# Performance work log

Measured on AMD Instinct MI355X. Metric: run time of the kernel, lower is better.

## Reference

```python
import jax, jax.numpy as jnp
import numpy as np

MAX_REL = 7  # maxRelativeDist

def _rel_pos_table(L, max_rel):
    # |i-j|, with distances beyond max_rel mapped to max_rel + log2(d - max_rel), clipped to [0, 2*max_rel]
    idx = jnp.arange(L)
    d = jnp.abs(idx[:, None] - idx[None, :]).astype(jnp.float32)
    far = d > max_rel
    d = jnp.where(far, max_rel + jnp.log2(jnp.maximum(d - max_rel, 1.0)), d)
    return jnp.clip(d, 0, 2 * max_rel).astype(jnp.int32)  # [L, L]

def setup_inputs() -> dict:
    key = jax.random.key(0)
    ks = jax.random.split(key, 16)
    B, L, C, P, H, DK = 8, 2048, 512, 64, 8, 64
    s = 0.02
    inp = {
        'qx': jax.random.normal(ks[0], (B, L, C), jnp.float32),
        'kx': jax.random.normal(ks[1], (B, L, C), jnp.float32),
        'vx': jax.random.normal(ks[2], (B, L, C), jnp.float32),
        'maskPAD': jnp.ones((B, L, L), jnp.int32),
        # pseudoAttn: Linear(C, P)
        'Wp': jax.random.normal(ks[3], (C, P), jnp.float32) * s,
        'bp': jnp.zeros((P,), jnp.float32),
        # WQ/WK: Linear(C, dkEnhance*DK*H) with dkEnhance=1
        'Wq': jax.random.normal(ks[4], (C, H * DK), jnp.float32) * s,
        'bq': jnp.zeros((H * DK,), jnp.float32),
        'Wk': jax.random.normal(ks[5], (C, H * DK), jnp.float32) * s,
        'bk': jnp.zeros((H * DK,), jnp.float32),
        'Wv': jax.random.normal(ks[6], (C, H * DK), jnp.float32) * s,
        'bv': jnp.zeros((H * DK,), jnp.float32),
        'Wo': jax.random.normal(ks[7], (H * DK, C), jnp.float32) * s,
        'bo': jnp.zeros((C,), jnp.float32),
        # relative position embeddings: [2*MAX_REL+1, H]
        'embK': jax.random.normal(ks[8], (2 * MAX_REL + 1, H), jnp.float32) * s,
        'embB': jax.random.normal(ks[9], (2 * MAX_REL + 1, H), jnp.float32) * s,
    }
    return inp

def reference(qx, kx, vx, maskPAD, Wp, bp, Wq, bq, Wk, bk, Wv, bv, Wo, bo, embK, embB):
    # dropout is identity (eval mode); preScores=None
    B, L, C = qx.shape
    H = embK.shape[1]
    DK = Wv.shape[1] // H
    P = Wp.shape[1]

    # pseudo-token compression
    pScore = vx @ Wp + bp                                   # [B, L, P]
    mask = (maskPAD[:, 0] == 0)[:, :, None]                 # [B, L, 1]
    pScore = jnp.where(mask, jnp.float32(-2.0 ** 15), pScore)
    pAlpha = jax.nn.softmax(pScore, axis=1)                 # softmax over L
    kxc = jnp.einsum('blp,blc->bpc', pAlpha, kx)            # [B, P, C]
    vxc = jnp.einsum('blp,blc->bpc', pAlpha, vx)            # [B, P, C]
    pAlpha_d = jax.lax.stop_gradient(pAlpha)

    # multi-head projections
    q = (qx @ Wq + bq).reshape(B, L, H, DK)                 # [B, L, H, DK]
    k = (kxc @ Wk + bk).reshape(B, P, H, DK)
    v = (vxc @ Wv + bv).reshape(B, P, H, DK)

    scores = jnp.einsum('blhd,bphd->bhlp', q, k) / np.sqrt(DK)  # [B, H, L, P]

    # relative-position modulation
    relTab = _rel_pos_table(L, MAX_REL)                     # [L, L] int
    Kmat = jnp.transpose(embK[relTab], (2, 1, 0))           # [H, L, L]
    Bmat = jnp.transpose(embB[relTab], (2, 1, 0))           # [H, L, L]
    Kterm = jnp.einsum('hlm,bmp->bhlp', Kmat, pAlpha_d)
    Bterm = jnp.einsum('hlm,bmp->bhlp', Bmat, pAlpha_d)
    scores = scores * Kterm + Bterm

    alpha = jax.nn.softmax(scores, axis=3)                  # over pseudo tokens
    z = jnp.einsum('bhlp,bphd->blhd', alpha, v).reshape(B, L, H * DK)
    z = z @ Wo + bo                                         # [B, L, C]
    return z, pScore, scores
```

## Files before the change

kernel.cpp:

```cpp
#include <hip/hip_runtime.h>


typedef __attribute__((ext_vector_type(8))) short bhalf8;
typedef __attribute__((ext_vector_type(4))) float fx4;

__device__ __forceinline__ unsigned short f2bf(float f) {
  union { float f; unsigned u; } v; v.f = f;
  unsigned u = v.u + 0x7fffu + ((v.u >> 16) & 1u);
  return (unsigned short)(u >> 16);
}
__device__ __forceinline__ float bf2f(unsigned short h) {
  union { unsigned u; float f; } v; v.u = ((unsigned)h) << 16;
  return v.f;
}
__device__ __forceinline__ void gld16(const void* g, void* l) {
  __builtin_amdgcn_global_load_lds(
      (const __attribute__((address_space(1))) void*)g,
      (__attribute__((address_space(3))) void*)l, 16, 0, 0);
}

template <int BM, int BN, int CMODE, int AF32, int KSPLIT>
__device__ __forceinline__ void gemm_body(
    int bxx, int byy, int bzz, char* smemc,
    const void* __restrict__ Av, const unsigned short* __restrict__ BT,
    const float* __restrict__ bias, void* __restrict__ Cout,
    int K, int lda, int ldbt, int ldc, int HDIV,
    long sAb, long sAh, long sBb, long sBh, long sCb, long sCh, long sCk,
    const int* __restrict__ mpad, float* __restrict__ aux)
{
  constexpr int NA = BM / 16, NB = BN / 16, NT = NA + NB;
  constexpr int WM = BM / 2, WN = BN / 2, FM = WM / 16, FN = WN / 16;
  unsigned short* lds = (unsigned short*)smemc;
  const int t = threadIdx.x, l = t & 63, w = t >> 6;
  const int wr = w >> 1, wc = w & 1;
  const int zz = bzz, b = zz / HDIV, h = zz % HDIV;
  const int row0 = KSPLIT ? 0 : byy * BM;
  const int koff = KSPLIT ? byy * K : 0;
  const long cko = KSPLIT ? (long)byy * sCk : 0;
  const int col0 = bxx * BN;
  const unsigned short* Ag = (const unsigned short*)Av + b * sAb + h * sAh + (long)row0 * lda + koff;
  const float* AgF = (const float*)Av + b * sAb + h * sAh + (long)row0 * lda + koff;
  const unsigned short* Bg = BT + b * sBb + h * sBh + (long)col0 * ldbt + koff;
  const int lr = l & 15, lc = l >> 4;

  fx4 acc[FM][FN];
#pragma unroll
  for (int i = 0; i < FM; ++i)
#pragma unroll
    for (int j = 0; j < FN; ++j) acc[i][j] = fx4{0.f, 0.f, 0.f, 0.f};

  for (int k0 = 0; k0 < K; k0 += 32) {
#pragma unroll
    for (int i = 0; i < NT / 4; ++i) {
      const int tile = w + i * 4;
      if constexpr (AF32 == 1) {
        if (tile < NA) {
          const float* gf = AgF + (long)(tile * 16 + lr) * lda + k0 + lc * 8;
          float4 x = *(const float4*)gf, y = *(const float4*)(gf + 4);
          bhalf8 pk;
          pk[0] = (short)f2bf(x.x); pk[1] = (short)f2bf(x.y);
          pk[2] = (short)f2bf(x.z); pk[3] = (short)f2bf(x.w);
          pk[4] = (short)f2bf(y.x); pk[5] = (short)f2bf(y.y);
          pk[6] = (short)f2bf(y.z); pk[7] = (short)f2bf(y.w);
          *(bhalf8*)&lds[tile * 512 + l * 8] = pk;
        } else {
          gld16(Bg + (long)((tile - NA) * 16 + lr) * ldbt + k0 + lc * 8, &lds[tile * 512]);
        }
      } else if constexpr (AF32 == 2) {
        if (tile < NA) {
          const float* gf = (const float*)Av + (long)zz * sAb + (long)byy * 131072
                            + (long)(tile * 16 + lr) * 512 + k0 + lc * 8;
          float4 x = make_float4(0.f, 0.f, 0.f, 0.f), y = x;
#pragma unroll
          for (int c = 0; c < 4; ++c) {
            float4 a = *(const float4*)(gf + (long)c * 32768);
            float4 bq = *(const float4*)(gf + (long)c * 32768 + 4);
            x.x += a.x; x.y += a.y; x.z += a.z; x.w += a.w;
            y.x += bq.x; y.y += bq.y; y.z += bq.z; y.w += bq.w;
          }
          bhalf8 pk;
          pk[0] = (short)f2bf(x.x); pk[1] = (short)f2bf(x.y);
          pk[2] = (short)f2bf(x.z); pk[3] = (short)f2bf(x.w);
          pk[4] = (short)f2bf(y.x); pk[5] = (short)f2bf(y.y);
          pk[6] = (short)f2bf(y.z); pk[7] = (short)f2bf(y.w);
          *(bhalf8*)&lds[tile * 512 + l * 8] = pk;
        } else {
          gld16(Bg + (long)((tile - NA) * 16 + lr) * ldbt + k0 + lc * 8, &lds[tile * 512]);
        }
      } else {
        const unsigned short* g = (tile < NA)
            ? Ag + (long)(tile * 16 + lr) * lda + k0 + lc * 8
            : Bg + (long)((tile - NA) * 16 + lr) * ldbt + k0 + lc * 8;
        gld16(g, &lds[tile * 512]);
      }
    }
    __syncthreads();
    bhalf8 af[FM], bf[FN];
#pragma unroll
    for (int i = 0; i < FM; ++i) af[i] = *(const bhalf8*)&lds[(wr * FM + i) * 512 + l * 8];
#pragma unroll
    for (int j = 0; j < FN; ++j) bf[j] = *(const bhalf8*)&lds[(NA + wc * FN + j) * 512 + l * 8];
#pragma unroll
    for (int i = 0; i < FM; ++i)
#pragma unroll
      for (int j = 0; j < FN; ++j)
        acc[i][j] = __builtin_amdgcn_mfma_f32_16x16x32_bf16(af[i], bf[j], acc[i][j], 0, 0, 0);
    __syncthreads();
  }

  if constexpr (CMODE == 3) {
    float (*tbuf)[65] = (float(*)[65])(smemc + NT * 1024);
#pragma unroll
    for (int fm = 0; fm < FM; ++fm) {
#pragma unroll
      for (int fn = 0; fn < FN; ++fn) {
        const int rg0 = row0 + wr * WM + fm * 16 + lc * 4;
        const int cg = col0 + wc * WN + fn * 16 + lr;
        const float bb = bias[cg];
#pragma unroll
        for (int jj = 0; jj < 4; ++jj) {
          const int rg = rg0 + jj;
          float vv = acc[fm][fn][jj] + bb;
          if (mpad[((long)(rg >> 11)) * (2048L * 2048) + (rg & 2047)] == 0) vv = -32768.f;
          __builtin_nontemporal_store(vv, (float*)Cout + (long)rg * ldc + cg);
          tbuf[rg - row0][cg] = vv;
        }
      }
    }
    __syncthreads();
    const int b0 = row0 >> 11, l0b = row0 & 2047;
    const int pp = t >> 2, li0 = (t & 3) * 16;
    float* dst = aux + ((long)b0 * 64 + pp) * 2048 + l0b + li0;
#pragma unroll
    for (int i = 0; i < 16; i += 4) {
      float4 o = make_float4(tbuf[li0 + i][pp],     tbuf[li0 + i + 1][pp],
                             tbuf[li0 + i + 2][pp], tbuf[li0 + i + 3][pp]);
      *(float4*)(dst + i) = o;
    }
  } else {
#pragma unroll
    for (int fm = 0; fm < FM; ++fm) {
#pragma unroll
      for (int fn = 0; fn < FN; ++fn) {
        const int rg0 = row0 + wr * WM + fm * 16 + lc * 4;
        const int cg = col0 + wc * WN + fn * 16 + lr;
        float bb = 0.f;
        if constexpr (CMODE == 4) {
          bb = (zz == 0) ? bias[cg] : ((const float*)mpad)[cg];
        } else {
          bb = bias ? bias[cg] : 0.f;
        }
#pragma unroll
        for (int jj = 0; jj < 4; ++jj) {
          const int rg = rg0 + jj;
          const float v = acc[fm][fn][jj] + bb;
          if constexpr (CMODE == 0) {
            ((float*)Cout)[b * sCb + h * sCh + cko + (long)rg * ldc + cg] = v;
          } else if constexpr (CMODE == 1) {
            ((unsigned short*)Cout)[b * sCb + h * sCh + (long)rg * ldc + cg] = f2bf(v);
          } else if constexpr (CMODE == 2) {
            ((unsigned short*)Cout)[(((long)(rg >> 6) * 8 + (cg >> 6)) * 64 + (cg & 63)) * 64 + (rg & 63)] = f2bf(v);
          } else if constexpr (CMODE == 4) {
            if (zz == 0)
              ((unsigned short*)Cout)[(long)rg * ldc + cg] = f2bf(v);
            else
              ((unsigned short*)Cout)[262144 + (((long)(rg >> 6) * 8 + (cg >> 6)) * 64 + (cg & 63)) * 64 + (rg & 63)] = f2bf(v);
          } else {
            __builtin_nontemporal_store(v, (float*)Cout + b * sCb + h * sCh + cko + (long)rg * ldc + cg);
          }
        }
      }
    }
  }
}

template <int BM, int BN, int CMODE, int AF32, int KSPLIT>
__global__ __launch_bounds__(256)
void gemm_mfma(const void* __restrict__ Av, const unsigned short* __restrict__ BT,
               const float* __restrict__ bias, void* __restrict__ Cout,
               int K, int lda, int ldbt, int ldc, int HDIV,
               long sAb, long sAh, long sBb, long sBh, long sCb, long sCh, long sCk,
               const int* __restrict__ mpad, float* __restrict__ aux)
{
  constexpr int SM = (BM / 16 + BN / 16) * 1024 + (CMODE == 3 ? 16640 : 0);
  __shared__ __align__(16) char smem[SM];
  gemm_body<BM, BN, CMODE, AF32, KSPLIT>(blockIdx.x, blockIdx.y, blockIdx.z, smem,
      Av, BT, bias, Cout, K, lda, ldbt, ldc, HDIV,
      sAb, sAh, sBb, sBh, sCb, sCh, sCk, mpad, aux);
}

__device__ __forceinline__ void kb_body(int bx, int by, char* smemc,
    const unsigned short* __restrict__ PSb,
    const float* __restrict__ embK, const float* __restrict__ embB,
    ushort2* __restrict__ KB)
{
  const int L = 2048, STR = 338;
  unsigned short* psw = (unsigned short*)smemc;
  float (*eKs)[8] = (float(*)[8])(smemc + 43264);
  float (*eBs)[8] = (float(*)[8])(smemc + 43264 + 512);
  const int t = threadIdx.x, b = by, l0 = bx * 64;
  if (t < 128) {
    int r = t >> 3, h = t & 7;
    eKs[r][h] = (r < 15) ? embK[r * 8 + h] : 0.f;
    eBs[r][h] = (r < 15) ? embB[r * 8 + h] : 0.f;
  }
  const int W0 = l0 - 136;
  const int w = t >> 6, ln = t & 63;
  for (int pr = w * 16; pr < w * 16 + 16; ++pr) {
    const unsigned short* src = PSb + ((long)b * 64 + pr) * 2048;
#pragma unroll
    for (int pass = 0; pass < 6; ++pass) {
      int j = pass * 64 + ln;
      if (j < 337) {
        int g = (j == 336) ? (L - 1) : (W0 + j);
        g = g < 0 ? 0 : (g > L - 1 ? L - 1 : g);
        psw[pr * STR + j] = src[g];
      }
    }
  }
  __syncthreads();
  const int p = ln;
  const int Btab[14] = {0,1,2,3,4,5,6,8,10,14,22,38,70,134};
  for (int step = 0; step < 16; ++step) {
    const int l = l0 + w * 16 + step;
    float U[15];
#pragma unroll
    for (int r = 0; r < 14; ++r) {
      int hi = l + Btab[r]; hi = hi > L - 1 ? L - 1 : hi;
      float u = bf2f(psw[p * STR + (hi - W0)]);
      const int lo = l - 1 - Btab[r];
      if (lo >= 0) u -= bf2f(psw[p * STR + (lo - W0)]);
      U[r] = u;
    }
    U[14] = bf2f(psw[p * STR + 336]);
    for (int h = 0; h < 8; ++h) {
      float Kt = 0.f, Bt = 0.f;
#pragma unroll
      for (int r = 0; r < 15; ++r) {
        Kt = fmaf(eKs[r][h] - eKs[r + 1][h], U[r], Kt);
        Bt = fmaf(eBs[r][h] - eBs[r + 1][h], U[r], Bt);
      }
      ushort2 o; o.x = f2bf(Kt); o.y = f2bf(Bt);
      KB[(((long)(b * 8 + h)) * L + l) * 64 + p] = o;
    }
  }
}

__global__ __launch_bounds__(256)
void combo1(const unsigned short* __restrict__ pAbf, const unsigned short* __restrict__ kxT,
            float* __restrict__ pbuf,
            const unsigned short* __restrict__ PSb,
            const float* __restrict__ embK, const float* __restrict__ embB,
            ushort2* __restrict__ KB)
{
  __shared__ __align__(16) char smem[44544];
  const int id = blockIdx.x;
  if (id < 256) {
    gemm_body<64, 128, 0, 0, 1>(id & 3, (id >> 2) & 3, id >> 4, smem,
        pAbf, kxT, nullptr, pbuf, 512, 2048, 2048, 512, 2,
        131072, 0, 1048576, 8388608, 131072, 1048576, 32768, nullptr, nullptr);
  } else {
    const int r = id - 256;
    kb_body(r & 31, r >> 5, smem, PSb, embK, embB, KB);
  }
}

__global__ __launch_bounds__(256)
void combo2(const float* __restrict__ pbuf, const unsigned short* __restrict__ WkT,
            const float* __restrict__ bk, const float* __restrict__ bv,
            unsigned short* __restrict__ kp,
            const float* __restrict__ qx, const unsigned short* __restrict__ WqT,
            const float* __restrict__ bq, unsigned short* __restrict__ qbf)
{
  __shared__ __align__(16) char smem[16384];
  const int id = blockIdx.x;
  if (id < 64) {
    gemm_body<64, 128, 4, 2, 0>(id & 3, (id >> 2) & 7, id >> 5, smem,
        pbuf, WkT, bk, kp, 512, 512, 512, 512, 1,
        1048576, 0, 262144, 0, 0, 0, 0, (const int*)bv, nullptr);
  } else {
    const int r = id - 64;
    gemm_body<128, 128, 1, 1, 0>(r & 3, r >> 2, 0, smem,
        qx, WqT, bq, qbf, 512, 512, 512, 512, 1,
        0, 0, 0, 0, 0, 0, 0, nullptr, nullptr);
  }
}

__device__ __forceinline__ void tr_body(float (*tile)[65], const float* __restrict__ in,
                                        unsigned short* __restrict__ out,
                                        int R, int Cd, int r0, int c0, int t)
{
  const int tr = t >> 4, tc4 = (t & 15) * 4;
#pragma unroll
  for (int pass = 0; pass < 4; ++pass) {
    int r = pass * 16 + tr;
    float4 v = *(const float4*)(in + (long)(r0 + r) * Cd + c0 + tc4);
    tile[r][tc4] = v.x; tile[r][tc4 + 1] = v.y; tile[r][tc4 + 2] = v.z; tile[r][tc4 + 3] = v.w;
  }
  __syncthreads();
#pragma unroll
  for (int pass = 0; pass < 4; ++pass) {
    int c = pass * 16 + tr;
    ushort4 o;
    o.x = f2bf(tile[tc4][c]);     o.y = f2bf(tile[tc4 + 1][c]);
    o.z = f2bf(tile[tc4 + 2][c]); o.w = f2bf(tile[tc4 + 3][c]);
    *(ushort4*)(out + (long)(c0 + c) * R + r0 + tc4) = o;
  }
}

__global__ __launch_bounds__(256)
void tconv_prep(const float* Wq, const float* Wk, const float* Wv, const float* Wo, const float* Wp,
                const float* kx, const float* vx,
                unsigned short* WqT, unsigned short* WkT, unsigned short* WvT,
                unsigned short* WoT, unsigned short* WpT,
                unsigned short* kxT, unsigned short* vxT)
{
  __shared__ float tile[64][65];
  const int z = blockIdx.z;
  const long LC = 2048L * 512;
  const float* in; unsigned short* out; int R, Cd;
  if (z < 5) {
    if (blockIdx.y >= 8) return;
    R = 512;
    switch (z) {
      case 0: in = Wq; out = WqT; Cd = 512; break;
      case 1: in = Wk; out = WkT; Cd = 512; break;
      case 2: in = Wv; out = WvT; Cd = 512; break;
      case 3: in = Wo; out = WoT; Cd = 512; break;
      default: in = Wp; out = WpT; Cd = 64; break;
    }
    if ((int)blockIdx.x * 64 >= Cd) return;
  } else {
    const int zz = z - 5;
    in = (zz < 8) ? kx + zz * LC : vx + (zz - 8) * LC;
    out = (zz < 8) ? kxT + zz * LC : vxT + (zz - 8) * LC;
    R = 2048; Cd = 512;
  }
  tr_body(tile, in, out, R, Cd, blockIdx.y * 64, blockIdx.x * 64, threadIdx.x);
}

__global__ __launch_bounds__(256)
void softmax_scan(const float* __restrict__ pScoreT,
                  unsigned short* __restrict__ PSb, unsigned short* __restrict__ pA_bf)
{
  __shared__ float red[256];
  const int p = blockIdx.x, b = blockIdx.y, t = threadIdx.x;
  const float* row = pScoreT + ((size_t)b * 64 + p) * 2048;
  float4 va = ((const float4*)row)[t * 2], vb = ((const float4*)row)[t * 2 + 1];
  float v[8] = {va.x, va.y, va.z, va.w, vb.x, vb.y, vb.z, vb.w};
  float mx = v[0];
#pragma unroll
  for (int i = 1; i < 8; ++i) mx = fmaxf(mx, v[i]);
  red[t] = mx; __syncthreads();
  for (int s = 128; s > 0; s >>= 1) { if (t < s) red[t] = fmaxf(red[t], red[t + s]); __syncthreads(); }
  float m = red[0]; __syncthreads();
  float e[8]; float s = 0.f;
#pragma unroll
  for (int i = 0; i < 8; ++i) { e[i] = expf(v[i] - m); s += e[i]; }
  red[t] = s; __syncthreads();
  for (int o = 1; o < 256; o <<= 1) {
    float x = (t >= o) ? red[t - o] : 0.f;
    __syncthreads(); red[t] += x; __syncthreads();
  }
  float inv = 1.0f / red[255];
  float run = red[t] - s;
  size_t base = ((size_t)b * 64 + p) * 2048 + (size_t)t * 8;
#pragma unroll
  for (int i = 0; i < 8; ++i) {
    run += e[i];
    PSb[base + i] = f2bf(run * inv);
    pA_bf[base + i] = f2bf(e[i] * inv);
  }
}

__global__ __launch_bounds__(256)
void attn_fused(const unsigned short* __restrict__ qb,
                const unsigned short* __restrict__ kp,
                const unsigned short* __restrict__ vpT,
                const ushort2* __restrict__ KB,
                float* __restrict__ sc_out,
                unsigned short* __restrict__ zpre)
{
  const int L = 2048;
  __shared__ __align__(16) unsigned short stg[24 * 512];
  unsigned short* qkb = &stg[8 * 512];
  const int t = threadIdx.x, l = t & 63, w = t >> 6, lr = l & 15, lc = l >> 4;
  const int flat = blockIdx.y * 16 + blockIdx.x;
  const int swz = (flat & 7) * 128 + (flat >> 3);
  const int z = swz >> 4, b = z >> 3, h = z & 7;
  const int l0 = (swz & 15) * 128;
  const unsigned short* Ag = qb + ((long)(b * L + l0)) * 512 + h * 64;
  const unsigned short* Bg = kp + (long)b * 64 * 512 + h * 64;
#pragma unroll
  for (int i = 0; i < 6; ++i) {
    const int tile = w + i * 4;
    const unsigned short* g;
    if (tile < 16) { int rt = tile >> 1, ks = tile & 1; g = Ag + (long)(rt * 16 + lr) * 512 + ks * 32 + lc * 8; }
    else { int j = tile - 16; int rt = j >> 1, ks = j & 1; g = Bg + (long)(rt * 16 + lr) * 512 + ks * 32 + lc * 8; }
    gld16(g, &stg[tile * 512]);
  }
  const ushort2* kbb = KB + (((long)(b * 8 + h)) * L + l0) * 64 + l;
  unsigned int kbreg[32];
#pragma unroll
  for (int i = 0; i < 32; ++i)
    kbreg[i] = *(const unsigned int*)(kbb + ((long)(w * 32 + i)) * 64);
  __syncthreads();
  const int wr = w >> 1, wc = w & 1;
  fx4 acc[4][2];
#pragma unroll
  for (int i = 0; i < 4; ++i)
#pragma unroll
    for (int j = 0; j < 2; ++j) acc[i][j] = fx4{0.f, 0.f, 0.f, 0.f};
#pragma unroll
  for (int ks = 0; ks < 2; ++ks) {
    bhalf8 af[4], bf[2];
#pragma unroll
    for (int i = 0; i < 4; ++i) af[i] = *(const bhalf8*)&stg[((wr * 4 + i) * 2 + ks) * 512 + l * 8];
#pragma unroll
    for (int j = 0; j < 2; ++j) bf[j] = *(const bhalf8*)&stg[(16 + (wc * 2 + j) * 2 + ks) * 512 + l * 8];
#pragma unroll
    for (int i = 0; i < 4; ++i)
#pragma unroll
      for (int j = 0; j < 2; ++j)
        acc[i][j] = __builtin_amdgcn_mfma_f32_16x16x32_bf16(af[i], bf[j], acc[i][j], 0, 0, 0);
  }
  __syncthreads();
#pragma unroll
  for (int fm = 0; fm < 4; ++fm)
#pragma unroll
    for (int fn = 0; fn < 2; ++fn)
#pragma unroll
      for (int jj = 0; jj < 4; ++jj) {
        const int row = wr * 64 + fm * 16 + lc * 4 + jj;
        const int col = wc * 32 + fn * 16 + lr;
        *(unsigned short*)((char*)qkb + ((row * 128 + col * 2) ^ ((row & 7) << 4))) = f2bf(acc[fm][fn][jj]);
      }
  __syncthreads();
  {
    const unsigned short* Vg = vpT + ((long)(b * 8 + h)) * 64 * 64;
#pragma unroll
    for (int i = 0; i < 2; ++i) {
      const int tile = w + i * 4, rt = tile >> 1, ks = tile & 1;
      gld16(Vg + (long)(rt * 16 + lr) * 64 + ks * 32 + lc * 8, &stg[tile * 512]);
    }
  }
  const int p = l;
  float* scb = sc_out + ((long)(b * 8 + h) * L + l0) * 64 + p;
#pragma unroll
  for (int c = 0; c < 8; ++c) {
    const int rbase = w * 32 + c * 4;
    float sv[4];
#pragma unroll
    for (int il = 0; il < 4; ++il) {
      const int row = rbase + il;
      const unsigned int kbw = kbreg[c * 4 + il];
      const float qkv = bf2f(*(const unsigned short*)((const char*)qkb + ((row * 128 + p * 2) ^ ((row & 7) << 4))));
      sv[il] = qkv * 0.125f * bf2f((unsigned short)(kbw & 0xffffu)) + bf2f((unsigned short)(kbw >> 16));
      __builtin_nontemporal_store(sv[il], scb + (long)row * 64);
    }
    float mx[4] = {sv[0], sv[1], sv[2], sv[3]};
#pragma unroll
    for (int o = 32; o > 0; o >>= 1)
#pragma unroll
      for (int il = 0; il < 4; ++il) mx[il] = fmaxf(mx[il], __shfl_xor(mx[il], o, 64));
    float ex[4], sm[4];
#pragma unroll
    for (int il = 0; il < 4; ++il) { ex[il] = __expf(sv[il] - mx[il]); sm[il] = ex[il]; }
#pragma unroll
    for (int o = 32; o > 0; o >>= 1)
#pragma unroll
      for (int il = 0; il < 4; ++il) sm[il] += __shfl_xor(sm[il], o, 64);
#pragma unroll
    for (int il = 0; il < 4; ++il) {
      const int row = rbase + il;
      *(unsigned short*)((char*)qkb + ((row * 128 + p * 2) ^ ((row & 7) << 4))) = f2bf(ex[il] / sm[il]);
    }
  }
  __syncthreads();
  fx4 a2[4][2];
#pragma unroll
  for (int i = 0; i < 4; ++i)
#pragma unroll
    for (int j = 0; j < 2; ++j) a2[i][j] = fx4{0.f, 0.f, 0.f, 0.f};
#pragma unroll
  for (int ks = 0; ks < 2; ++ks) {
    bhalf8 paf[4], pvf[2];
#pragma unroll
    for (int i = 0; i < 4; ++i) {
      const int row = (wr * 4 + i) * 16 + lr;
      paf[i] = *(const bhalf8*)((const char*)qkb + ((row * 128 + ks * 64 + lc * 16) ^ ((row & 7) << 4)));
    }
#pragma unroll
    for (int j = 0; j < 2; ++j)
      pvf[j] = *(const bhalf8*)&stg[(((wc * 2 + j) * 2 + ks) * 512) + l * 8];
#pragma unroll
    for (int i = 0; i < 4; ++i)
#pragma unroll
      for (int j = 0; j < 2; ++j)
        a2[i][j] = __builtin_amdgcn_mfma_f32_16x16x32_bf16(paf[i], pvf[j], a2[i][j], 0, 0, 0);
  }
#pragma unroll
  for (int fm = 0; fm < 4; ++fm)
#pragma unroll
    for (int fn = 0; fn < 2; ++fn)
#pragma unroll
      for (int jj = 0; jj < 4; ++jj) {
        const int row = wr * 64 + fm * 16 + lc * 4 + jj;
        const int col = wc * 32 + fn * 16 + lr;
        zpre[((long)(b * L + l0 + row)) * 512 + h * 64 + col] = f2bf(a2[fm][fn][jj]);
      }
}

extern "C" void kernel_launch(void* const* d_in, const int* in_sizes, int n_in,
                              void* d_out, int out_size, void* d_ws, size_t ws_size,
                              hipStream_t stream)
{
  const int B = 8, L = 2048, C = 512, P = 64;
  const float* qx = (const float*)d_in[0];
  const float* kx = (const float*)d_in[1];
  const float* vx = (const float*)d_in[2];
  const int* maskPAD = (const int*)d_in[3];
  const float* Wp = (const float*)d_in[4];
  const float* bp = (const float*)d_in[5];
  const float* Wq = (const float*)d_in[6];
  const float* bq = (const float*)d_in[7];
  const float* Wk = (const float*)d_in[8];
  const float* bk = (const float*)d_in[9];
  const float* Wv = (const float*)d_in[10];
  const float* bv = (const float*)d_in[11];
  const float* Wo = (const float*)d_in[12];
  const float* bo = (const float*)d_in[13];
  const float* embK = (const float*)d_in[14];
  const float* embB = (const float*)d_in[15];

  float* z_out  = (float*)d_out;
  float* ps_out = z_out + (size_t)B * L * C;
  float* sc_out = ps_out + (size_t)B * L * P;

  char* w8 = (char*)d_ws;
  size_t o = 0;
  auto take = [&](size_t n) { char* r = w8 + o; o += n; return r; };
  unsigned short* R_A  = (unsigned short*)take(16777216);
  unsigned short* R_B  = (unsigned short*)take(16777216);
  unsigned short* kxT  = (unsigned short*)take(16777216);
  unsigned short* vxT  = (unsigned short*)take(16777216);
  unsigned short* WqT  = (unsigned short*)take(524288);
  unsigned short* WkT  = (unsigned short*)take(524288);
  unsigned short* WvT  = (unsigned short*)take(524288);
  unsigned short* WoT  = (unsigned short*)take(524288);
  unsigned short* WpT  = (unsigned short*)take(65536);
  float* pScoreT       = (float*)take(4194304);
  unsigned short* PSb  = (unsigned short*)take(2097152);
  unsigned short* pAbf = (unsigned short*)take(2097152);
  float* pbuf          = (float*)take(8388608);
  unsigned short* kp   = (unsigned short*)take(1048576);
  ushort2* KB          = (ushort2*)take(33554432);

  tconv_prep<<<dim3(8, 32, 21), 256, 0, stream>>>(
      Wq, Wk, Wv, Wo, Wp, kx, vx, WqT, WkT, WvT, WoT, WpT, kxT, vxT);
  gemm_mfma<64, 64, 3, 1, 0><<<dim3(1, 256, 1), 256, 0, stream>>>(
      vx, WpT, bp, ps_out, 512, 512, 512, 64, 1, 0, 0, 0, 0, 0, 0, 0, maskPAD, pScoreT);
  softmax_scan<<<dim3(P, B), 256, 0, stream>>>(pScoreT, PSb, pAbf);
  combo1<<<dim3(512), 256, 0, stream>>>(pAbf, kxT, pbuf, PSb, embK, embB, KB);
  combo2<<<dim3(576), 256, 0, stream>>>(pbuf, WkT, bk, bv, kp, qx, WqT, bq, R_B);
  attn_fused<<<dim3(16, 64), 256, 0, stream>>>(
      R_B, kp, kp + 262144, KB, sc_out, R_A);
  gemm_mfma<128, 128, 5, 0, 0><<<dim3(4, 128, 1), 256, 0, stream>>>(
      R_A, WoT, bo, z_out, 512, 512, 512, 512, 1, 0, 0, 0, 0, 0, 0, 0, nullptr, nullptr);
}
```

Baseline: 201.5 us.

## Merge transpose prep and pScore GEMM into one launch, shrink combo1 GEMM tiles

Folds the transpose/convert prep kernel and the pScore GEMM into a single combo0 launch. The GEMM now reads the fp32 Wp directly, with strided loads and bf16 conversion, so the separate WpT transpose is no longer needed. The pAlpha·kx GEMM in combo1 moves from 64x128 to 64x64 tiles, doubling its block count to raise parallelism. This removes one launch and one serial dependency, in exchange for uncoalesced scalar B loads in the pScore GEMM and smaller tiles with less reuse. The grid of 4616 includes 8 idle blocks past id 4608.

```diff
diff --git a/kernel.cpp b/kernel.cpp
--- a/kernel.cpp
+++ b/kernel.cpp
@@ -19,14 +19,15 @@
       (__attribute__((address_space(3))) void*)l, 16, 0, 0);
 }
 
-template <int BM, int BN, int CMODE, int AF32, int KSPLIT>
+template <int BM, int BN, int CMODE, int AF32, int KSPLIT, int BF32>
 __device__ __forceinline__ void gemm_body(
     int bxx, int byy, int bzz, char* smemc,
     const void* __restrict__ Av, const unsigned short* __restrict__ BT,
     const float* __restrict__ bias, void* __restrict__ Cout,
     int K, int lda, int ldbt, int ldc, int HDIV,
     long sAb, long sAh, long sBb, long sBh, long sCb, long sCh, long sCk,
-    const int* __restrict__ mpad, float* __restrict__ aux)
+    const int* __restrict__ mpad, float* __restrict__ aux,
+    const float* __restrict__ Bf32)
 {
   constexpr int NA = BM / 16, NB = BN / 16, NT = NA + NB;
   constexpr int WM = BM / 2, WN = BN / 2, FM = WM / 16, FN = WN / 16;
@@ -53,6 +54,7 @@
 #pragma unroll
     for (int i = 0; i < NT / 4; ++i) {
       const int tile = w + i * 4;
+      bool handled = false;
       if constexpr (AF32 == 1) {
         if (tile < NA) {
           const float* gf = AgF + (long)(tile * 16 + lr) * lda + k0 + lc * 8;
@@ -63,8 +65,7 @@
           pk[4] = (short)f2bf(y.x); pk[5] = (short)f2bf(y.y);
           pk[6] = (short)f2bf(y.z); pk[7] = (short)f2bf(y.w);
           *(bhalf8*)&lds[tile * 512 + l * 8] = pk;
-        } else {
-          gld16(Bg + (long)((tile - NA) * 16 + lr) * ldbt + k0 + lc * 8, &lds[tile * 512]);
+          handled = true;
         }
       } else if constexpr (AF32 == 2) {
         if (tile < NA) {
@@ -84,14 +85,23 @@
           pk[4] = (short)f2bf(y.x); pk[5] = (short)f2bf(y.y);
           pk[6] = (short)f2bf(y.z); pk[7] = (short)f2bf(y.w);
           *(bhalf8*)&lds[tile * 512 + l * 8] = pk;
+          handled = true;
+        }
+      }
+      if (!handled) {
+        if constexpr (BF32 == 1) {
+          const int ct = tile - NA;
+          const float* gfB = Bf32 + (long)(k0 + lc * 8) * ldbt + col0 + ct * 16 + lr;
+          bhalf8 pk;
+#pragma unroll
+          for (int i2 = 0; i2 < 8; ++i2) pk[i2] = (short)f2bf(gfB[(long)i2 * ldbt]);
+          *(bhalf8*)&lds[tile * 512 + l * 8] = pk;
         } else {
-          gld16(Bg + (long)((tile - NA) * 16 + lr) * ldbt + k0 + lc * 8, &lds[tile * 512]);
+          const unsigned short* g = (tile < NA)
+              ? Ag + (long)(tile * 16 + lr) * lda + k0 + lc * 8
+              : Bg + (long)((tile - NA) * 16 + lr) * ldbt + k0 + lc * 8;
+          gld16(g, &lds[tile * 512]);
         }
-      } else {
-        const unsigned short* g = (tile < NA)
-            ? Ag + (long)(tile * 16 + lr) * lda + k0 + lc * 8
-            : Bg + (long)((tile - NA) * 16 + lr) * ldbt + k0 + lc * 8;
-        gld16(g, &lds[tile * 512]);
       }
     }
     __syncthreads();
@@ -184,9 +194,69 @@
 {
   constexpr int SM = (BM / 16 + BN / 16) * 1024 + (CMODE == 3 ? 16640 : 0);
   __shared__ __align__(16) char smem[SM];
-  gemm_body<BM, BN, CMODE, AF32, KSPLIT>(blockIdx.x, blockIdx.y, blockIdx.z, smem,
+  gemm_body<BM, BN, CMODE, AF32, KSPLIT, 0>(blockIdx.x, blockIdx.y, blockIdx.z, smem,
       Av, BT, bias, Cout, K, lda, ldbt, ldc, HDIV,
-      sAb, sAh, sBb, sBh, sCb, sCh, sCk, mpad, aux);
+      sAb, sAh, sBb, sBh, sCb, sCh, sCk, mpad, aux, nullptr);
+}
+
+__device__ __forceinline__ void tr_body(float (*tile)[65], const float* __restrict__ in,
+                                        unsigned short* __restrict__ out,
+                                        int R, int Cd, int r0, int c0, int t)
+{
+  const int tr = t >> 4, tc4 = (t & 15) * 4;
+#pragma unroll
+  for (int pass = 0; pass < 4; ++pass) {
+    int r = pass * 16 + tr;
+    float4 v = *(const float4*)(in + (long)(r0 + r) * Cd + c0 + tc4);
+    tile[r][tc4] = v.x; tile[r][tc4 + 1] = v.y; tile[r][tc4 + 2] = v.z; tile[r][tc4 + 3] = v.w;
+  }
+  __syncthreads();
+#pragma unroll
+  for (int pass = 0; pass < 4; ++pass) {
+    int c = pass * 16 + tr;
+    ushort4 o;
+    o.x = f2bf(tile[tc4][c]);     o.y = f2bf(tile[tc4 + 1][c]);
+    o.z = f2bf(tile[tc4 + 2][c]); o.w = f2bf(tile[tc4 + 3][c]);
+    *(ushort4*)(out + (long)(c0 + c) * R + r0 + tc4) = o;
+  }
+}
+
+__global__ __launch_bounds__(256)
+void combo0(const float* __restrict__ vx, const float* __restrict__ Wp,
+            const float* __restrict__ bp, const int* __restrict__ maskPAD,
+            float* __restrict__ ps_out, float* __restrict__ pScoreT,
+            const float* __restrict__ kx,
+            const float* __restrict__ Wq, const float* __restrict__ Wk,
+            const float* __restrict__ Wv, const float* __restrict__ Wo,
+            unsigned short* __restrict__ kxT, unsigned short* __restrict__ vxT,
+            unsigned short* __restrict__ WqT, unsigned short* __restrict__ WkT,
+            unsigned short* __restrict__ WvT, unsigned short* __restrict__ WoT)
+{
+  __shared__ __align__(16) char smem[24832];
+  const int id = blockIdx.x;
+  const long LC = 2048L * 512;
+  if (id < 256) {
+    gemm_body<64, 64, 3, 1, 0, 1>(0, id, 0, smem,
+        vx, nullptr, bp, ps_out, 512, 512, 64, 64, 1,
+        0, 0, 0, 0, 0, 0, 0, maskPAD, pScoreT, Wp);
+  } else if (id < 4352) {
+    const int r = id - 256;
+    const int zz = r >> 8, rem = r & 255;
+    const float* in = (zz < 8) ? kx + zz * LC : vx + (zz - 8) * LC;
+    unsigned short* out = (zz < 8) ? kxT + zz * LC : vxT + (zz - 8) * LC;
+    tr_body((float(*)[65])smem, in, out, 2048, 512, (rem >> 3) * 64, (rem & 7) * 64, threadIdx.x);
+  } else if (id < 4608) {
+    const int r = id - 4352;
+    const int z = r >> 6, rem = r & 63;
+    const float* in; unsigned short* out;
+    switch (z) {
+      case 0: in = Wq; out = WqT; break;
+      case 1: in = Wk; out = WkT; break;
+      case 2: in = Wv; out = WvT; break;
+      default: in = Wo; out = WoT; break;
+    }
+    tr_body((float(*)[65])smem, in, out, 512, 512, (rem >> 3) * 64, (rem & 7) * 64, threadIdx.x);
+  }
 }
 
 __device__ __forceinline__ void kb_body(int bx, int by, char* smemc,
@@ -255,12 +325,12 @@
 {
   __shared__ __align__(16) char smem[44544];
   const int id = blockIdx.x;
-  if (id < 256) {
-    gemm_body<64, 128, 0, 0, 1>(id & 3, (id >> 2) & 3, id >> 4, smem,
+  if (id < 512) {
+    gemm_body<64, 64, 0, 0, 1, 0>(id & 7, (id >> 3) & 3, id >> 5, smem,
         pAbf, kxT, nullptr, pbuf, 512, 2048, 2048, 512, 2,
-        131072, 0, 1048576, 8388608, 131072, 1048576, 32768, nullptr, nullptr);
+        131072, 0, 1048576, 8388608, 131072, 1048576, 32768, nullptr, nullptr, nullptr);
   } else {
-    const int r = id - 256;
+    const int r = id - 512;
     kb_body(r & 31, r >> 5, smem, PSb, embK, embB, KB);
   }
 }
@@ -275,68 +345,15 @@
   __shared__ __align__(16) char smem[16384];
   const int id = blockIdx.x;
   if (id < 64) {
-    gemm_body<64, 128, 4, 2, 0>(id & 3, (id >> 2) & 7, id >> 5, smem,
+    gemm_body<64, 128, 4, 2, 0, 0>(id & 3, (id >> 2) & 7, id >> 5, smem,
         pbuf, WkT, bk, kp, 512, 512, 512, 512, 1,
-        1048576, 0, 262144, 0, 0, 0, 0, (const int*)bv, nullptr);
+        1048576, 0, 262144, 0, 0, 0, 0, (const int*)bv, nullptr, nullptr);
   } else {
     const int r = id - 64;
-    gemm_body<128, 128, 1, 1, 0>(r & 3, r >> 2, 0, smem,
+    gemm_body<128, 128, 1, 1, 0, 0>(r & 3, r >> 2, 0, smem,
         qx, WqT, bq, qbf, 512, 512, 512, 512, 1,
-        0, 0, 0, 0, 0, 0, 0, nullptr, nullptr);
-  }
-}
-
-__device__ __forceinline__ void tr_body(float (*tile)[65], const float* __restrict__ in,
-                                        unsigned short* __restrict__ out,
-                                        int R, int Cd, int r0, int c0, int t)
-{
-  const int tr = t >> 4, tc4 = (t & 15) * 4;
-#pragma unroll
-  for (int pass = 0; pass < 4; ++pass) {
-    int r = pass * 16 + tr;
-    float4 v = *(const float4*)(in + (long)(r0 + r) * Cd + c0 + tc4);
-    tile[r][tc4] = v.x; tile[r][tc4 + 1] = v.y; tile[r][tc4 + 2] = v.z; tile[r][tc4 + 3] = v.w;
-  }
-  __syncthreads();
-#pragma unroll
-  for (int pass = 0; pass < 4; ++pass) {
-    int c = pass * 16 + tr;
-    ushort4 o;
-    o.x = f2bf(tile[tc4][c]);     o.y = f2bf(tile[tc4 + 1][c]);
-    o.z = f2bf(tile[tc4 + 2][c]); o.w = f2bf(tile[tc4 + 3][c]);
-    *(ushort4*)(out + (long)(c0 + c) * R + r0 + tc4) = o;
-  }
-}
-
-__global__ __launch_bounds__(256)
-void tconv_prep(const float* Wq, const float* Wk, const float* Wv, const float* Wo, const float* Wp,
-                const float* kx, const float* vx,
-                unsigned short* WqT, unsigned short* WkT, unsigned short* WvT,
-                unsigned short* WoT, unsigned short* WpT,
-                unsigned short* kxT, unsigned short* vxT)
-{
-  __shared__ float tile[64][65];
-  const int z = blockIdx.z;
-  const long LC = 2048L * 512;
-  const float* in; unsigned short* out; int R, Cd;
-  if (z < 5) {
-    if (blockIdx.y >= 8) return;
-    R = 512;
-    switch (z) {
-      case 0: in = Wq; out = WqT; Cd = 512; break;
-      case 1: in = Wk; out = WkT; Cd = 512; break;
-      case 2: in = Wv; out = WvT; Cd = 512; break;
-      case 3: in = Wo; out = WoT; Cd = 512; break;
-      default: in = Wp; out = WpT; Cd = 64; break;
-    }
-    if ((int)blockIdx.x * 64 >= Cd) return;
-  } else {
-    const int zz = z - 5;
-    in = (zz < 8) ? kx + zz * LC : vx + (zz - 8) * LC;
-    out = (zz < 8) ? kxT + zz * LC : vxT + (zz - 8) * LC;
-    R = 2048; Cd = 512;
-  }
-  tr_body(tile, in, out, R, Cd, blockIdx.y * 64, blockIdx.x * 64, threadIdx.x);
+        0, 0, 0, 0, 0, 0, 0, nullptr, nullptr, nullptr);
+  }
 }
 
 __global__ __launch_bounds__(256)
@@ -548,7 +565,6 @@
   unsigned short* WkT  = (unsigned short*)take(524288);
   unsigned short* WvT  = (unsigned short*)take(524288);
   unsigned short* WoT  = (unsigned short*)take(524288);
-  unsigned short* WpT  = (unsigned short*)take(65536);
   float* pScoreT       = (float*)take(4194304);
   unsigned short* PSb  = (unsigned short*)take(2097152);
   unsigned short* pAbf = (unsigned short*)take(2097152);
@@ -556,12 +572,11 @@
   unsigned short* kp   = (unsigned short*)take(1048576);
   ushort2* KB          = (ushort2*)take(33554432);
 
-  tconv_prep<<<dim3(8, 32, 21), 256, 0, stream>>>(
-      Wq, Wk, Wv, Wo, Wp, kx, vx, WqT, WkT, WvT, WoT, WpT, kxT, vxT);
-  gemm_mfma<64, 64, 3, 1, 0><<<dim3(1, 256, 1), 256, 0, stream>>>(
-      vx, WpT, bp, ps_out, 512, 512, 512, 64, 1, 0, 0, 0, 0, 0, 0, 0, maskPAD, pScoreT);
+  combo0<<<dim3(4616), 256, 0, stream>>>(
+      vx, Wp, bp, maskPAD, ps_out, pScoreT, kx,
+      Wq, Wk, Wv, Wo, kxT, vxT, WqT, WkT, WvT, WoT);
   softmax_scan<<<dim3(P, B), 256, 0, stream>>>(pScoreT, PSb, pAbf);
-  combo1<<<dim3(512), 256, 0, stream>>>(pAbf, kxT, pbuf, PSb, embK, embB, KB);
+  combo1<<<dim3(768), 256, 0, stream>>>(pAbf, kxT, pbuf, PSb, embK, embB, KB);
   combo2<<<dim3(576), 256, 0, stream>>>(pbuf, WkT, bk, bv, kp, qx, WqT, bq, R_B);
   attn_fused<<<dim3(16, 64), 256, 0, stream>>>(
       R_B, kp, kp + 262144, KB, sc_out, R_A);
```

Result: no change. 200.9 us (-0.3%).
